# Performance work log

Hardware: AMD Instinct MI355X
Metric: run time of the kernel (lower is better)

## Reference

```python
import jax, jax.numpy as jnp
import numpy as np

EMBED_DIM = 1024
NUM_HEADS = 16
HEAD_DIM = EMBED_DIM // NUM_HEADS
KERNEL = 3
PAD = KERNEL // 2
B, L = 4, 1024


def conv1d(x, w, b):
    # x: [B, D, L], w: [D_out, D_in, K], b: [D_out]; 'same' padding like nn.Conv1d(padding=K//2)
    y = jax.lax.conv_general_dilated(
        x, w, window_strides=(1,), padding=[(PAD, PAD)],
        dimension_numbers=('NCH', 'OIH', 'NCH'))
    return y + b[None, :, None]


def setup_inputs() -> dict:
    key = jax.random.key(0)
    ks = jax.random.split(key, 12)
    fan = EMBED_DIM * KERNEL
    bound = 1.0 / np.sqrt(fan)
    def wconv(k):
        return jax.random.uniform(k, (EMBED_DIM, EMBED_DIM, KERNEL), jnp.float32, -bound, bound)
    def bconv(k):
        return jax.random.uniform(k, (EMBED_DIM,), jnp.float32, -bound, bound)
    return {
        'query': jax.random.normal(ks[0], (B, L, EMBED_DIM), jnp.float32),
        'key': jax.random.normal(ks[1], (B, L, EMBED_DIM), jnp.float32),
        'value': jax.random.normal(ks[2], (B, L, EMBED_DIM), jnp.float32),
        'key_padding_mask': jax.random.randint(ks[3], (B, L), 0, 2) > 0,
        'attn_mask': jnp.zeros((L, L), jnp.float32),
        'q_w': wconv(ks[4]), 'q_b': bconv(ks[5]),
        'k_w': wconv(ks[6]), 'k_b': bconv(ks[7]),
        'v_w': wconv(ks[8]), 'v_b': bconv(ks[9]),
        'o_w': wconv(ks[10]), 'o_b': bconv(ks[11]),
    }


def reference(query, key, value, key_padding_mask, attn_mask,
              q_w, q_b, k_w, k_b, v_w, v_b, o_w, o_b):
    scale = HEAD_DIM ** -0.5
    # projections: [B, D, L]
    q = conv1d(jnp.swapaxes(query, 1, 2), q_w, q_b)
    k = conv1d(jnp.swapaxes(key, 1, 2), k_w, k_b)
    v = conv1d(jnp.swapaxes(value, 1, 2), v_w, v_b)
    # [B, H, d, L]
    q = q.reshape(B, NUM_HEADS, HEAD_DIM, L)
    k = k.reshape(B, NUM_HEADS, HEAD_DIM, L)
    v = v.reshape(B, NUM_HEADS, HEAD_DIM, L)
    # scores: [B, H, L, L]
    scores = jnp.einsum('bhdi,bhdj->bhij', q, k) * scale
    scores = scores + attn_mask[None, None, :, :]
    scores = jnp.where(key_padding_mask[:, None, None, :], -jnp.inf, scores)
    attn = jax.nn.softmax(scores, axis=-1)  # dropout p=0 (eval) -> identity
    out = jnp.einsum('bhij,bhdj->bhdi', attn, v)  # [B, H, d, L]
    out = out.reshape(B, EMBED_DIM, L)
    out = conv1d(out, o_w, o_b)
    return jnp.swapaxes(out, 1, 2)  # [B, L, D]
```

## Files before the change

### kernel.cpp

```cpp
#include <hip/hip_runtime.h>
#include <math.h>

#define NB 4
#define NL 1024
#define ND 1024
#define NH 16
#define HD 64
#define PLN 4194304

typedef __attribute__((ext_vector_type(8))) short bf16x8;
typedef __attribute__((ext_vector_type(4))) float f32x4;

static __device__ __forceinline__ unsigned short f32_to_bf16(float f) {
  unsigned u = __float_as_uint(f);
  u += 0x7FFFu + ((u >> 16) & 1u);
  return (unsigned short)(u >> 16);
}
static __device__ __forceinline__ float bf16_to_f32(unsigned short s) {
  return __uint_as_float(((unsigned)s) << 16);
}
static __device__ __forceinline__ float exp2_f(float x) {
  float r;
  asm("v_exp_f32 %0, %1" : "=v"(r) : "v"(x));
  return r;
}

static __device__ __forceinline__ void split8(float4 a, float4 b, bf16x8* hi, bf16x8* lo) {
  unsigned u[8] = {__float_as_uint(a.x), __float_as_uint(a.y),
                   __float_as_uint(a.z), __float_as_uint(a.w),
                   __float_as_uint(b.x), __float_as_uint(b.y),
                   __float_as_uint(b.z), __float_as_uint(b.w)};
  union { unsigned p[4]; bf16x8 v; } H, L;
#pragma unroll
  for (int p = 0; p < 4; ++p) {
    unsigned u0 = u[2 * p], u1 = u[2 * p + 1];
    H.p[p] = __builtin_amdgcn_perm(u1, u0, 0x07060302u);
    unsigned l0 = __float_as_uint(__uint_as_float(u0) - __uint_as_float(u0 & 0xFFFF0000u));
    unsigned l1 = __float_as_uint(__uint_as_float(u1) - __uint_as_float(u1 & 0xFFFF0000u));
    L.p[p] = __builtin_amdgcn_perm(l1, l0, 0x07060302u);
  }
  *hi = H.v; *lo = L.v;
}

__global__ __launch_bounds__(256) void wcvt_kernel(
    const float* __restrict__ w0, const float* __restrict__ w1,
    const float* __restrict__ w2, const float* __restrict__ w3,
    unsigned short* __restrict__ wb, int* __restrict__ flag)
{
  if (blockIdx.x == 0 && blockIdx.y == 0 && threadIdx.x == 0) flag[0] = 0;
  const int t = blockIdx.y;
  const int o = blockIdx.x;
  const float* w = (t == 0) ? w0 : (t == 1) ? w1 : (t == 2) ? w2 : w3;
  unsigned short* hi = wb + (size_t)t * 6 * (1u << 20);
  unsigned short* lo = hi + 3 * (1u << 20);
  const int tid = threadIdx.x;
  float v[12];
  const float* src = w + (size_t)o * (ND * 3) + tid * 12;
#pragma unroll
  for (int j = 0; j < 3; ++j) {
    float4 f = *(const float4*)(src + j * 4);
    v[j * 4 + 0] = f.x; v[j * 4 + 1] = f.y; v[j * 4 + 2] = f.z; v[j * 4 + 3] = f.w;
  }
#pragma unroll
  for (int k = 0; k < 3; ++k) {
    unsigned short hh[4], ll[4];
#pragma unroll
    for (int ii = 0; ii < 4; ++ii) {
      float x = v[ii * 3 + k];
      unsigned short h = f32_to_bf16(x);
      float r = x - bf16_to_f32(h);
      hh[ii] = h; ll[ii] = f32_to_bf16(r);
    }
    size_t dst = (size_t)k * (ND * ND) + (size_t)o * ND + tid * 4;
    *(ushort4*)&hi[dst] = make_ushort4(hh[0], hh[1], hh[2], hh[3]);
    *(ushort4*)&lo[dst] = make_ushort4(ll[0], ll[1], ll[2], ll[3]);
  }
}

__global__ __launch_bounds__(256) void amask_scan(
    const float* __restrict__ a, int* __restrict__ flag)
{
  size_t i = ((size_t)blockIdx.x * 256 + threadIdx.x) * 4;
  float4 v = *(const float4*)&a[i];
  if (v.x != 0.f || v.y != 0.f || v.z != 0.f || v.w != 0.f) atomicOr(flag, 1);
}

__global__ __launch_bounds__(256) void xsplit_kernel(
    const float* __restrict__ x0, const float* __restrict__ x1,
    const float* __restrict__ x2, unsigned short* __restrict__ xs)
{
  const int z = blockIdx.y;
  const float* x = (z == 0) ? x0 : (z == 1) ? x1 : x2;
  const size_t i = ((size_t)blockIdx.x * 256 + threadIdx.x) * 8;
  float4 a = *(const float4*)&x[i];
  float4 b = *(const float4*)&x[i + 4];
  bf16x8 hi, lo;
  split8(a, b, &hi, &lo);
  unsigned short* ph = xs + (size_t)z * 2 * PLN;
  *(bf16x8*)&ph[i] = hi;
  *(bf16x8*)&ph[PLN + i] = lo;
}

template<int ASPLIT, int MODE>
__global__ __launch_bounds__(256, 3) void conv_mfma2(
    const void* X0v, const void* X1v, const void* X2v,
    const unsigned short* __restrict__ wb,
    const float* b0, const float* b1, const float* b2,
    float* Y0)
{
  __shared__ __align__(16) unsigned char Araw[16384];
  __shared__ unsigned short Bh[128 * 32];
  __shared__ unsigned short Bl[128 * 32];
  float* Af = (float*)Araw;
  unsigned short* Ah = (unsigned short*)Araw;
  unsigned short* Al = (unsigned short*)(Araw + 8192);

  const int tid = threadIdx.x, lane = tid & 63, wave = tid >> 6;
  const int lin = blockIdx.x + 8 * (blockIdx.y + 32 * blockIdx.z);
  const int g = lin & 7, t = lin >> 3;
  const int nb = (g & 3) * 2 + (t & 1);
  const int mb = (g >> 2) * 16 + ((t >> 1) & 15);
  const int z  = t >> 5;
  const int n0 = nb * 128, m0 = mb * 128;
  const int b = m0 >> 10, l0v = m0 & (NL - 1);

  const unsigned short* Wh = (MODE == 0) ? wb + (size_t)z * 6 * (1u << 20) : wb;
  const unsigned short* Wl = Wh + 3 * (1u << 20);

  const float* Xf = nullptr;
  const unsigned short* Xh_ = nullptr;
  const unsigned short* Xl_ = nullptr;
  if (ASPLIT) {
    const unsigned short* p = (const unsigned short*)((MODE == 0)
        ? (z == 0 ? X0v : (z == 1 ? X1v : X2v)) : X0v);
    Xh_ = p; Xl_ = p + PLN;
  } else {
    Xf = (const float*)((MODE == 0) ? (z == 0 ? X0v : (z == 1 ? X1v : X2v)) : X0v);
  }

  const int wm = (wave >> 1) * 64, wn = (wave & 1) * 64;
  const int mrow = lane & 15, quad = lane >> 4;
  const int r16 = lane >> 2, cs = lane & 3;
  const int src_chunk = (cs - (r16 >> 1)) & 3;
  const int bswz = ((quad + (mrow >> 1)) & 3) * 8;

  f32x4 acc[4][4] = {};

  const int kbeg = (MODE == 0) ? 0 : z;
  const int kend = (MODE == 0) ? 3 : z + 1;
  for (int koff = kbeg; koff < kend; ++koff) {
    const bool edge_lo = (l0v == 0 && koff == 0);
    const bool edge_hi = (l0v == NL - 128 && koff == 2);
    for (int i0 = 0; i0 < ND; i0 += 32) {
#pragma unroll
      for (int s = 0; s < 2; ++s) {
        const int seg = wave * 2 + s;
        const size_t goff = ((size_t)koff << 20) +
                            (size_t)(n0 + seg * 16 + r16) * ND + i0 + src_chunk * 8;
        __builtin_amdgcn_global_load_lds(
            (const __attribute__((address_space(1))) unsigned int*)(Wh + goff),
            (__attribute__((address_space(3))) unsigned int*)&Bh[seg * 512], 16, 0, 0);
        __builtin_amdgcn_global_load_lds(
            (const __attribute__((address_space(1))) unsigned int*)(Wl + goff),
            (__attribute__((address_space(3))) unsigned int*)&Bl[seg * 512], 16, 0, 0);
      }
      if (ASPLIT) {
#pragma unroll
        for (int j = 0; j < 4; ++j) {
          const int seg = wave * 2 + (j & 1);
          const int row = seg * 16 + (lane >> 2);
          const int slot = lane & 3;
          const int chunk = (slot - (row >> 1)) & 3;
          int l = l0v + row + koff - 1;
          l = (l < 0) ? 0 : (l > NL - 1 ? NL - 1 : l);
          const unsigned short* Xp = (j >> 1) ? Xl_ : Xh_;
          unsigned short* dst = ((j >> 1) ? Al : Ah) + seg * 512;
          const unsigned short* gp = Xp + ((size_t)(b << 10) + l) * ND + i0 + chunk * 8;
          __builtin_amdgcn_global_load_lds(
              (const __attribute__((address_space(1))) unsigned int*)gp,
              (__attribute__((address_space(3))) unsigned int*)dst, 16, 0, 0);
        }
      } else {
#pragma unroll
        for (int j = 0; j < 4; ++j) {
          const int s = (wave * 4 + j) * 64 + lane;
          const int row = s >> 3, sir = s & 7;
          const int chunk = (sir - (row & 7)) & 7;
          int l = l0v + row + koff - 1;
          l = (l < 0) ? 0 : (l > NL - 1 ? NL - 1 : l);
          const float* gp = Xf + ((size_t)(b << 10) + l) * ND + i0 + chunk * 4;
          __builtin_amdgcn_global_load_lds(
              (const __attribute__((address_space(1))) unsigned int*)gp,
              (__attribute__((address_space(3))) unsigned int*)&Af[(wave * 4 + j) * 256],
              16, 0, 0);
        }
      }
      __syncthreads();
      if (edge_lo || edge_hi) {
        const int er = edge_lo ? 0 : 127;
        if (ASPLIT) {
          if (tid < 16) {
            unsigned short* pl = (tid < 8) ? Ah : Al;
            *(ushort4*)&pl[er * 32 + (tid & 7) * 4] = make_ushort4(0, 0, 0, 0);
          }
        } else {
          if (tid < 8) *(float4*)&Af[er * 32 + tid * 4] = make_float4(0.f, 0.f, 0.f, 0.f);
        }
        __syncthreads();
      }
      bf16x8 ah[4], al[4];
      if (ASPLIT) {
#pragma unroll
        for (int mi = 0; mi < 4; ++mi) {
          const int row = wm + mi * 16 + mrow;
          const int cso = ((quad + (row >> 1)) & 3) * 8;
          ah[mi] = *(const bf16x8*)&Ah[row * 32 + cso];
          al[mi] = *(const bf16x8*)&Al[row * 32 + cso];
        }
      } else {
#pragma unroll
        for (int mi = 0; mi < 4; ++mi) {
          const int row = wm + mi * 16 + mrow, r7 = row & 7;
          float4 fa = *(const float4*)&Af[row * 32 + (((quad * 2) + r7) & 7) * 4];
          float4 fb = *(const float4*)&Af[row * 32 + (((quad * 2 + 1) + r7) & 7) * 4];
          split8(fa, fb, &ah[mi], &al[mi]);
        }
      }
#pragma unroll
      for (int ni = 0; ni < 4; ++ni) {
        const int brow = wn + ni * 16 + mrow;
        bf16x8 bh = *(const bf16x8*)&Bh[brow * 32 + bswz];
        bf16x8 bl = *(const bf16x8*)&Bl[brow * 32 + bswz];
#pragma unroll
        for (int mi = 0; mi < 4; ++mi) {
          acc[mi][ni] = __builtin_amdgcn_mfma_f32_16x16x32_bf16(ah[mi], bh, acc[mi][ni], 0, 0, 0);
          acc[mi][ni] = __builtin_amdgcn_mfma_f32_16x16x32_bf16(ah[mi], bl, acc[mi][ni], 0, 0, 0);
          acc[mi][ni] = __builtin_amdgcn_mfma_f32_16x16x32_bf16(al[mi], bh, acc[mi][ni], 0, 0, 0);
        }
      }
      __syncthreads();
    }
  }

  if (MODE == 0) {
    const float* bias = (z == 0) ? b0 : (z == 1) ? b1 : b2;
    unsigned short* U = (unsigned short*)Y0;
    if (z < 2) {
      unsigned short* Ph = U + (size_t)(2 * z) * PLN;
      unsigned short* Pl = Ph + PLN;
      const float sc = (z == 0) ? 0.18033688011112042f : 1.0f;
#pragma unroll
      for (int ni = 0; ni < 4; ++ni) {
        const int n = n0 + wn + ni * 16 + mrow;
        const float bv = bias[n];
        const int h = n >> 6, dd = n & 63;
        const int bh = b * NH + h;
#pragma unroll
        for (int mi = 0; mi < 4; ++mi) {
          const int mbase = m0 + wm + mi * 16 + quad * 4;
          f32x4 v = acc[mi][ni];
#pragma unroll
          for (int r = 0; r < 4; ++r) {
            const int l = (mbase + r) & (NL - 1);
            const float val = (v[r] + bv) * sc;
            const unsigned u = __float_as_uint(val);
            const unsigned short hh = (unsigned short)(u >> 16);
            const float res = val - __uint_as_float(u & 0xFFFF0000u);
            const unsigned short ll = (unsigned short)(__float_as_uint(res) >> 16);
            const size_t off = ((size_t)bh * NL + l) * HD + dd;
            Ph[off] = hh; Pl[off] = ll;
          }
        }
      }
    } else {
      unsigned short* Pv = U + (size_t)4 * PLN;
#pragma unroll
      for (int ni = 0; ni < 4; ++ni) {
        const int n = n0 + wn + ni * 16 + mrow;
        const float bv = bias[n];
        const int h = n >> 6, dd = n & 63;
        const int bh = b * NH + h;
#pragma unroll
        for (int mi = 0; mi < 4; ++mi) {
          const int mbase = m0 + wm + mi * 16 + quad * 4;
          const int lb = mbase & (NL - 1);
          f32x4 v = acc[mi][ni];
          ushort4 s4 = make_ushort4(f32_to_bf16(v[0] + bv), f32_to_bf16(v[1] + bv),
                                    f32_to_bf16(v[2] + bv), f32_to_bf16(v[3] + bv));
          *(ushort4*)&Pv[((size_t)bh * HD + dd) * NL + lb] = s4;
        }
      }
    }
  } else {
    float* P = Y0 + (size_t)z * ((size_t)NB * NL * ND);
#pragma unroll
    for (int ni = 0; ni < 4; ++ni) {
      const int n = n0 + wn + ni * 16 + mrow;
#pragma unroll
      for (int mi = 0; mi < 4; ++mi) {
        const int mbase = m0 + wm + mi * 16 + quad * 4;
        f32x4 v = acc[mi][ni];
#pragma unroll
        for (int r = 0; r < 4; ++r) {
          const int l = (mbase + r) & (NL - 1);
          P[((size_t)(b << 10) + l) * ND + n] = v[r];
        }
      }
    }
  }
}

__global__ __launch_bounds__(256) void reduce_kernel(
    const float* __restrict__ P, const float* __restrict__ bias, float* __restrict__ out)
{
  const size_t S = (size_t)NB * NL * ND;
  const size_t idx = ((size_t)blockIdx.x * 256 + threadIdx.x) * 4;
  const int n = (int)(idx & (ND - 1));
  float4 p0 = *(const float4*)&P[idx];
  float4 p1 = *(const float4*)&P[idx + S];
  float4 p2 = *(const float4*)&P[idx + 2 * S];
  float4 bv = *(const float4*)&bias[n];
  float4 r;
  r.x = p0.x + p1.x + p2.x + bv.x;
  r.y = p0.y + p1.y + p2.y + bv.y;
  r.z = p0.z + p1.z + p2.z + bv.z;
  r.w = p0.w + p1.w + p2.w + bv.w;
  *(float4*)&out[idx] = r;
}

__global__ __launch_bounds__(256, 3) void attn_mfma(
    const unsigned short* __restrict__ U, const int* __restrict__ kpm,
    const float* __restrict__ amask, const int* __restrict__ aflagp,
    unsigned short* __restrict__ AO)
{
  __shared__ __align__(16) unsigned short S[3 * 4096];
  __shared__ __align__(16) float Fm[NL];
  unsigned short* Kh = S;
  unsigned short* Kl = S + 4096;
  unsigned short* Vt = S + 8192;

  const int tid = threadIdx.x, lane = tid & 63, wave = tid >> 6;
  const int c = lane & 15, quad = lane >> 4;
  const int lin = blockIdx.x;
  const int bh = (lin & 7) + 8 * (lin >> 7);
  const int mt = (lin >> 3) & 15;
  const int b = bh >> 4;
  const int m0 = mt * 64;
  const int aflag = *aflagp;
  const int mrow = wave * 16 + c;
  const int gm = m0 + mrow;

  const size_t PLs = (size_t)PLN;
  const unsigned short* qTh = U;
  const unsigned short* qTl = U + PLs;
  const unsigned short* kTh = U + 2 * PLs;
  const unsigned short* kTl = U + 3 * PLs;
  const unsigned short* vTt = U + 4 * PLs;

  const int srow = lane >> 3;
  const int slot = lane & 7;
  const int chunk = (slot - srow) & 7;

#pragma unroll
  for (int q = 0; q < 4; ++q) {
    const int pl = q >> 1;
    const int i = wave * 2 + (q & 1);
    const int row = i * 8 + srow;
    const unsigned short* src = (pl ? qTl : qTh) +
        ((size_t)bh * NL + m0 + row) * HD + chunk * 8;
    unsigned short* dst = (pl ? Kl : Kh) + i * 512;
    __builtin_amdgcn_global_load_lds(
        (const __attribute__((address_space(1))) unsigned int*)src,
        (__attribute__((address_space(3))) unsigned int*)dst, 16, 0, 0);
  }
  {
    int4 kv = *(const int4*)&kpm[b * NL + tid * 4];
    float4 f;
    f.x = kv.x ? -INFINITY : 0.f;
    f.y = kv.y ? -INFINITY : 0.f;
    f.z = kv.z ? -INFINITY : 0.f;
    f.w = kv.w ? -INFINITY : 0.f;
    *(float4*)&Fm[tid * 4] = f;
  }
  __syncthreads();
  bf16x8 qbh[2], qbl[2];
#pragma unroll
  for (int kb = 0; kb < 2; ++kb) {
    const int cso = ((kb * 4 + quad + mrow) & 7) * 8;
    qbh[kb] = *(const bf16x8*)&Kh[mrow * 64 + cso];
    qbl[kb] = *(const bf16x8*)&Kl[mrow * 64 + cso];
  }

  f32x4 acc[4] = {};
  float m_r = -INFINITY, l_r = 0.0f;

  for (int n0t = 0; n0t < NL; n0t += 64) {
    __syncthreads();

#pragma unroll
    for (int q = 0; q < 6; ++q) {
      const int pl = q >> 1;
      const int i = wave * 2 + (q & 1);
      const int row = i * 8 + srow;
      const unsigned short* src;
      unsigned short* dst;
      if (pl == 0)      { src = kTh + ((size_t)bh * NL + n0t + row) * HD + chunk * 8; dst = Kh + i * 512; }
      else if (pl == 1) { src = kTl + ((size_t)bh * NL + n0t + row) * HD + chunk * 8; dst = Kl + i * 512; }
      else              { src = vTt + ((size_t)bh * HD + row) * NL + n0t + chunk * 8; dst = Vt + i * 512; }
      __builtin_amdgcn_global_load_lds(
          (const __attribute__((address_space(1))) unsigned int*)src,
          (__attribute__((address_space(3))) unsigned int*)dst, 16, 0, 0);
    }

    float mval[4][4];
#pragma unroll
    for (int nf = 0; nf < 4; ++nf) {
      float4 fm = *(const float4*)&Fm[n0t + nf * 16 + quad * 4];
      mval[nf][0] = fm.x; mval[nf][1] = fm.y; mval[nf][2] = fm.z; mval[nf][3] = fm.w;
    }
    if (aflag) {
#pragma unroll
      for (int nf = 0; nf < 4; ++nf)
#pragma unroll
        for (int r = 0; r < 4; ++r) {
          const int gn = n0t + nf * 16 + quad * 4 + r;
          mval[nf][r] += amask[(size_t)gm * NL + gn] * 1.4426950408889634f;
        }
    }
    __syncthreads();

    f32x4 sa[4] = {};
    __builtin_amdgcn_s_setprio(1);
#pragma unroll
    for (int kb = 0; kb < 2; ++kb)
#pragma unroll
      for (int nf = 0; nf < 4; ++nf) {
        const int row = nf * 16 + c;
        const int cso = ((kb * 4 + quad + row) & 7) * 8;
        bf16x8 kah = *(const bf16x8*)&Kh[row * 64 + cso];
        bf16x8 kal = *(const bf16x8*)&Kl[row * 64 + cso];
        sa[nf] = __builtin_amdgcn_mfma_f32_16x16x32_bf16(kah, qbh[kb], sa[nf], 0, 0, 0);
        sa[nf] = __builtin_amdgcn_mfma_f32_16x16x32_bf16(kah, qbl[kb], sa[nf], 0, 0, 0);
        sa[nf] = __builtin_amdgcn_mfma_f32_16x16x32_bf16(kal, qbh[kb], sa[nf], 0, 0, 0);
      }
    __builtin_amdgcn_s_setprio(0);

    float p[4][4];
    float tmax = -INFINITY;
#pragma unroll
    for (int nf = 0; nf < 4; ++nf)
#pragma unroll
      for (int r = 0; r < 4; ++r) {
        float s = sa[nf][r] + mval[nf][r];
        p[nf][r] = s;
        tmax = fmaxf(tmax, s);
      }
    tmax = fmaxf(tmax, __shfl_xor(tmax, 16));
    tmax = fmaxf(tmax, __shfl_xor(tmax, 32));
    float rs = 0.f;
    if (__all(tmax - m_r <= 8.0f)) {
      const float msafe = m_r;
#pragma unroll
      for (int nf = 0; nf < 4; ++nf)
#pragma unroll
        for (int r = 0; r < 4; ++r) {
          float e = exp2_f(p[nf][r] - msafe);
          p[nf][r] = e;
          rs += e;
        }
      rs += __shfl_xor(rs, 16);
      rs += __shfl_xor(rs, 32);
      l_r += rs;
    } else {
      const float newm = fmaxf(m_r, tmax);
      const float msafe = (newm == -INFINITY) ? 0.f : newm;
      const float alpha = exp2_f(m_r - msafe);
#pragma unroll
      for (int nf = 0; nf < 4; ++nf)
#pragma unroll
        for (int r = 0; r < 4; ++r) {
          float e = exp2_f(p[nf][r] - msafe);
          p[nf][r] = e;
          rs += e;
        }
      rs += __shfl_xor(rs, 16);
      rs += __shfl_xor(rs, 32);
      l_r = l_r * alpha + rs;
      m_r = newm;
#pragma unroll
      for (int df = 0; df < 4; ++df) {
        acc[df][0] *= alpha; acc[df][1] *= alpha;
        acc[df][2] *= alpha; acc[df][3] *= alpha;
      }
    }

    unsigned q16[4][2];
#pragma unroll
    for (int nf = 0; nf < 4; ++nf)
#pragma unroll
      for (int w = 0; w < 2; ++w)
        q16[nf][w] = (unsigned)f32_to_bf16(p[nf][2 * w]) |
                     ((unsigned)f32_to_bf16(p[nf][2 * w + 1]) << 16);

#pragma unroll
    for (int kb = 0; kb < 2; ++kb) {
      union { unsigned d[4]; bf16x8 v; } pb;
#pragma unroll
      for (int w = 0; w < 4; ++w) {
        const int addr = ((((quad & 1) * 2 + (w >> 1)) * 16 + c) << 2);
        unsigned v0 = __builtin_amdgcn_ds_bpermute(addr, (int)q16[2 * kb][w & 1]);
        unsigned v1 = __builtin_amdgcn_ds_bpermute(addr, (int)q16[2 * kb + 1][w & 1]);
        pb.d[w] = (quad >> 1) ? v1 : v0;
      }
      __builtin_amdgcn_s_setprio(1);
#pragma unroll
      for (int df = 0; df < 4; ++df) {
        const int row = df * 16 + c;
        const int cso = ((kb * 4 + quad + row) & 7) * 8;
        bf16x8 va = *(const bf16x8*)&Vt[row * 64 + cso];
        acc[df] = __builtin_amdgcn_mfma_f32_16x16x32_bf16(va, pb.v, acc[df], 0, 0, 0);
      }
      __builtin_amdgcn_s_setprio(0);
    }
  }

  __syncthreads();
  const float inv = 1.0f / l_r;
  float* Ob = (float*)S + wave * (16 * 68);
#pragma unroll
  for (int df = 0; df < 4; ++df)
#pragma unroll
    for (int r = 0; r < 4; ++r)
      Ob[c * 68 + df * 16 + quad * 4 + r] = acc[df][r] * inv;
  __syncthreads();
  const int mr2 = lane >> 2, cq2 = lane & 3;
  const int h = bh & 15;
  unsigned short* AOl_ = AO + PLN;
#pragma unroll
  for (int ii = 0; ii < 4; ++ii) {
    const int chunk2 = cq2 * 4 + ii;
    float4 v = *(const float4*)&Ob[mr2 * 68 + chunk2 * 4];
    const size_t off = ((size_t)(b << 10) + (m0 + wave * 16 + mr2)) * ND + h * HD + chunk2 * 4;
    float vv[4] = {v.x, v.y, v.z, v.w};
    ushort4 hh, ll;
    unsigned short* hp = (unsigned short*)&hh;
    unsigned short* lp = (unsigned short*)&ll;
#pragma unroll
    for (int e = 0; e < 4; ++e) {
      const unsigned u = __float_as_uint(vv[e]);
      hp[e] = (unsigned short)(u >> 16);
      const float res = vv[e] - __uint_as_float(u & 0xFFFF0000u);
      lp[e] = (unsigned short)(__float_as_uint(res) >> 16);
    }
    *(ushort4*)&AO[off] = hh;
    *(ushort4*)&AOl_[off] = ll;
  }
}

extern "C" void kernel_launch(void* const* d_in, const int* in_sizes, int n_in,
                              void* d_out, int out_size, void* d_ws, size_t ws_size,
                              hipStream_t stream) {
  (void)in_sizes; (void)n_in; (void)out_size;
  const float* query = (const float*)d_in[0];
  const float* key_  = (const float*)d_in[1];
  const float* value = (const float*)d_in[2];
  const int*   kpm   = (const int*)d_in[3];
  const float* amask = (const float*)d_in[4];
  const float* q_w = (const float*)d_in[5];
  const float* q_b = (const float*)d_in[6];
  const float* k_w = (const float*)d_in[7];
  const float* k_b = (const float*)d_in[8];
  const float* v_w = (const float*)d_in[9];
  const float* v_b = (const float*)d_in[10];
  const float* o_w = (const float*)d_in[11];
  const float* o_b = (const float*)d_in[12];
  float* out = (float*)d_out;

  unsigned short* Wb  = (unsigned short*)d_ws;
  unsigned short* U   = (unsigned short*)((char*)d_ws + (size_t)50331648);
  float*          P   = (float*)((char*)d_ws + (size_t)50331648);
  unsigned short* AOs = (unsigned short*)d_ws;
  unsigned short* Xs  = (unsigned short*)((char*)d_ws + (size_t)92274688);
  int* flag = (int*)d_out;
  const bool presplit = ws_size >= (size_t)142606336;

  wcvt_kernel<<<dim3(1024, 4), 256, 0, stream>>>(q_w, k_w, v_w, o_w, Wb, flag);
  amask_scan<<<1024, 256, 0, stream>>>(amask, flag);
  if (presplit) {
    xsplit_kernel<<<dim3(2048, 3), 256, 0, stream>>>(query, key_, value, Xs);
    conv_mfma2<1, 0><<<dim3(8, 32, 3), 256, 0, stream>>>(
        Xs, Xs + (size_t)2 * PLN, Xs + (size_t)4 * PLN, Wb, q_b, k_b, v_b, (float*)U);
  } else {
    conv_mfma2<0, 0><<<dim3(8, 32, 3), 256, 0, stream>>>(
        query, key_, value, Wb, q_b, k_b, v_b, (float*)U);
  }
  attn_mfma<<<1024, 256, 0, stream>>>(U, kpm, amask, flag, AOs);
  conv_mfma2<1, 1><<<dim3(8, 32, 3), 256, 0, stream>>>(
      AOs, AOs, AOs, Wb + (size_t)3 * 6 * (1u << 20), o_b, o_b, o_b, P);
  reduce_kernel<<<4096, 256, 0, stream>>>(P, o_b, out);
}
```

Measured before the change: 518.5 us.

## Double-buffer LDS tiles in conv and attention kernels to overlap loads

Both the conv GEMM kernel and the attention kernel now use two LDS buffers, so the global-to-LDS copy for the next tile is issued before computing on the current one. Each iteration needs one barrier instead of two. In the conv kernel the boundary-row zeroing moves from an LDS store plus extra barrier to register masking of the A fragments. The conv kernel's LDS doubles to 64KB and its launch bound drops from 3 to 2 blocks per CU, which lowers occupancy in exchange for the overlap.

```diff
diff --git a/kernel.cpp b/kernel.cpp
--- a/kernel.cpp
+++ b/kernel.cpp
@@ -102,18 +102,13 @@
 }
 
 template<int ASPLIT, int MODE>
-__global__ __launch_bounds__(256, 3) void conv_mfma2(
+__global__ __launch_bounds__(256, 2) void conv_mfma3(
     const void* X0v, const void* X1v, const void* X2v,
     const unsigned short* __restrict__ wb,
     const float* b0, const float* b1, const float* b2,
     float* Y0)
 {
-  __shared__ __align__(16) unsigned char Araw[16384];
-  __shared__ unsigned short Bh[128 * 32];
-  __shared__ unsigned short Bl[128 * 32];
-  float* Af = (float*)Araw;
-  unsigned short* Ah = (unsigned short*)Araw;
-  unsigned short* Al = (unsigned short*)(Araw + 8192);
+  __shared__ __align__(16) unsigned char LDSb[2][32768];
 
   const int tid = threadIdx.x, lane = tid & 63, wave = tid >> 6;
   const int lin = blockIdx.x + 8 * (blockIdx.y + 32 * blockIdx.z);
@@ -130,7 +125,7 @@
   const float* Xf = nullptr;
   const unsigned short* Xh_ = nullptr;
   const unsigned short* Xl_ = nullptr;
-  if (ASPLIT) {
+  if constexpr (ASPLIT) {
     const unsigned short* p = (const unsigned short*)((MODE == 0)
         ? (z == 0 ? X0v : (z == 1 ? X1v : X2v)) : X0v);
     Xh_ = p; Xl_ = p + PLN;
@@ -144,102 +139,115 @@
   const int src_chunk = (cs - (r16 >> 1)) & 3;
   const int bswz = ((quad + (mrow >> 1)) & 3) * 8;
 
+  const int NSTEP = (MODE == 0) ? 96 : 32;
+
+  auto stage = [&](int s, int buf) {
+    const int koff = (MODE == 0) ? (s >> 5) : z;
+    const int i0 = ((MODE == 0) ? (s & 31) : s) << 5;
+    unsigned short* BhD = (unsigned short*)(LDSb[buf] + 16384);
+    unsigned short* BlD = (unsigned short*)(LDSb[buf] + 24576);
+#pragma unroll
+    for (int s2 = 0; s2 < 2; ++s2) {
+      const int seg = wave * 2 + s2;
+      const size_t goff = ((size_t)koff << 20) +
+                          (size_t)(n0 + seg * 16 + r16) * ND + i0 + src_chunk * 8;
+      __builtin_amdgcn_global_load_lds(
+          (const __attribute__((address_space(1))) unsigned int*)(Wh + goff),
+          (__attribute__((address_space(3))) unsigned int*)&BhD[seg * 512], 16, 0, 0);
+      __builtin_amdgcn_global_load_lds(
+          (const __attribute__((address_space(1))) unsigned int*)(Wl + goff),
+          (__attribute__((address_space(3))) unsigned int*)&BlD[seg * 512], 16, 0, 0);
+    }
+    if constexpr (ASPLIT) {
+      unsigned short* AhD = (unsigned short*)(LDSb[buf]);
+      unsigned short* AlD = (unsigned short*)(LDSb[buf] + 8192);
+#pragma unroll
+      for (int j = 0; j < 4; ++j) {
+        const int seg = wave * 2 + (j & 1);
+        const int row = seg * 16 + (lane >> 2);
+        const int slot = lane & 3;
+        const int chunk = (slot - (row >> 1)) & 3;
+        int l = l0v + row + koff - 1;
+        l = (l < 0) ? 0 : (l > NL - 1 ? NL - 1 : l);
+        const unsigned short* Xp = (j >> 1) ? Xl_ : Xh_;
+        unsigned short* dst = ((j >> 1) ? AlD : AhD) + seg * 512;
+        const unsigned short* gp = Xp + ((size_t)(b << 10) + l) * ND + i0 + chunk * 8;
+        __builtin_amdgcn_global_load_lds(
+            (const __attribute__((address_space(1))) unsigned int*)gp,
+            (__attribute__((address_space(3))) unsigned int*)dst, 16, 0, 0);
+      }
+    } else {
+      float* AfD = (float*)(LDSb[buf]);
+#pragma unroll
+      for (int j = 0; j < 4; ++j) {
+        const int s2 = (wave * 4 + j) * 64 + lane;
+        const int row = s2 >> 3, sir = s2 & 7;
+        const int chunk = (sir - (row & 7)) & 7;
+        int l = l0v + row + koff - 1;
+        l = (l < 0) ? 0 : (l > NL - 1 ? NL - 1 : l);
+        const float* gp = Xf + ((size_t)(b << 10) + l) * ND + i0 + chunk * 4;
+        __builtin_amdgcn_global_load_lds(
+            (const __attribute__((address_space(1))) unsigned int*)gp,
+            (__attribute__((address_space(3))) unsigned int*)&AfD[(wave * 4 + j) * 256],
+            16, 0, 0);
+      }
+    }
+  };
+
   f32x4 acc[4][4] = {};
-
-  const int kbeg = (MODE == 0) ? 0 : z;
-  const int kend = (MODE == 0) ? 3 : z + 1;
-  for (int koff = kbeg; koff < kend; ++koff) {
-    const bool edge_lo = (l0v == 0 && koff == 0);
-    const bool edge_hi = (l0v == NL - 128 && koff == 2);
-    for (int i0 = 0; i0 < ND; i0 += 32) {
-#pragma unroll
-      for (int s = 0; s < 2; ++s) {
-        const int seg = wave * 2 + s;
-        const size_t goff = ((size_t)koff << 20) +
-                            (size_t)(n0 + seg * 16 + r16) * ND + i0 + src_chunk * 8;
-        __builtin_amdgcn_global_load_lds(
-            (const __attribute__((address_space(1))) unsigned int*)(Wh + goff),
-            (__attribute__((address_space(3))) unsigned int*)&Bh[seg * 512], 16, 0, 0);
-        __builtin_amdgcn_global_load_lds(
-            (const __attribute__((address_space(1))) unsigned int*)(Wl + goff),
-            (__attribute__((address_space(3))) unsigned int*)&Bl[seg * 512], 16, 0, 0);
-      }
-      if (ASPLIT) {
-#pragma unroll
-        for (int j = 0; j < 4; ++j) {
-          const int seg = wave * 2 + (j & 1);
-          const int row = seg * 16 + (lane >> 2);
-          const int slot = lane & 3;
-          const int chunk = (slot - (row >> 1)) & 3;
-          int l = l0v + row + koff - 1;
-          l = (l < 0) ? 0 : (l > NL - 1 ? NL - 1 : l);
-          const unsigned short* Xp = (j >> 1) ? Xl_ : Xh_;
-          unsigned short* dst = ((j >> 1) ? Al : Ah) + seg * 512;
-          const unsigned short* gp = Xp + ((size_t)(b << 10) + l) * ND + i0 + chunk * 8;
-          __builtin_amdgcn_global_load_lds(
-              (const __attribute__((address_space(1))) unsigned int*)gp,
-              (__attribute__((address_space(3))) unsigned int*)dst, 16, 0, 0);
-        }
-      } else {
-#pragma unroll
-        for (int j = 0; j < 4; ++j) {
-          const int s = (wave * 4 + j) * 64 + lane;
-          const int row = s >> 3, sir = s & 7;
-          const int chunk = (sir - (row & 7)) & 7;
-          int l = l0v + row + koff - 1;
-          l = (l < 0) ? 0 : (l > NL - 1 ? NL - 1 : l);
-          const float* gp = Xf + ((size_t)(b << 10) + l) * ND + i0 + chunk * 4;
-          __builtin_amdgcn_global_load_lds(
-              (const __attribute__((address_space(1))) unsigned int*)gp,
-              (__attribute__((address_space(3))) unsigned int*)&Af[(wave * 4 + j) * 256],
-              16, 0, 0);
-        }
-      }
-      __syncthreads();
-      if (edge_lo || edge_hi) {
-        const int er = edge_lo ? 0 : 127;
-        if (ASPLIT) {
-          if (tid < 16) {
-            unsigned short* pl = (tid < 8) ? Ah : Al;
-            *(ushort4*)&pl[er * 32 + (tid & 7) * 4] = make_ushort4(0, 0, 0, 0);
-          }
-        } else {
-          if (tid < 8) *(float4*)&Af[er * 32 + tid * 4] = make_float4(0.f, 0.f, 0.f, 0.f);
-        }
-        __syncthreads();
-      }
-      bf16x8 ah[4], al[4];
-      if (ASPLIT) {
-#pragma unroll
-        for (int mi = 0; mi < 4; ++mi) {
-          const int row = wm + mi * 16 + mrow;
-          const int cso = ((quad + (row >> 1)) & 3) * 8;
-          ah[mi] = *(const bf16x8*)&Ah[row * 32 + cso];
-          al[mi] = *(const bf16x8*)&Al[row * 32 + cso];
-        }
-      } else {
-#pragma unroll
-        for (int mi = 0; mi < 4; ++mi) {
-          const int row = wm + mi * 16 + mrow, r7 = row & 7;
-          float4 fa = *(const float4*)&Af[row * 32 + (((quad * 2) + r7) & 7) * 4];
-          float4 fb = *(const float4*)&Af[row * 32 + (((quad * 2 + 1) + r7) & 7) * 4];
-          split8(fa, fb, &ah[mi], &al[mi]);
-        }
-      }
-#pragma unroll
-      for (int ni = 0; ni < 4; ++ni) {
-        const int brow = wn + ni * 16 + mrow;
-        bf16x8 bh = *(const bf16x8*)&Bh[brow * 32 + bswz];
-        bf16x8 bl = *(const bf16x8*)&Bl[brow * 32 + bswz];
-#pragma unroll
-        for (int mi = 0; mi < 4; ++mi) {
-          acc[mi][ni] = __builtin_amdgcn_mfma_f32_16x16x32_bf16(ah[mi], bh, acc[mi][ni], 0, 0, 0);
-          acc[mi][ni] = __builtin_amdgcn_mfma_f32_16x16x32_bf16(ah[mi], bl, acc[mi][ni], 0, 0, 0);
-          acc[mi][ni] = __builtin_amdgcn_mfma_f32_16x16x32_bf16(al[mi], bh, acc[mi][ni], 0, 0, 0);
-        }
-      }
-      __syncthreads();
-    }
+  const bf16x8 zz = {};
+
+  stage(0, 0);
+  __syncthreads();
+  int cur = 0;
+  for (int s = 0; s < NSTEP; ++s) {
+    if (s + 1 < NSTEP) stage(s + 1, cur ^ 1);
+
+    const int koff = (MODE == 0) ? (s >> 5) : z;
+    const bool e_lo = (l0v == 0 && koff == 0);
+    const bool e_hi = (l0v == NL - 128 && koff == 2);
+
+    bf16x8 ah[4], al[4];
+    if constexpr (ASPLIT) {
+      const unsigned short* Ah = (const unsigned short*)(LDSb[cur]);
+      const unsigned short* Al = (const unsigned short*)(LDSb[cur] + 8192);
+#pragma unroll
+      for (int mi = 0; mi < 4; ++mi) {
+        const int row = wm + mi * 16 + mrow;
+        const int cso = ((quad + (row >> 1)) & 3) * 8;
+        ah[mi] = *(const bf16x8*)&Ah[row * 32 + cso];
+        al[mi] = *(const bf16x8*)&Al[row * 32 + cso];
+        const bool kill = (e_lo && row == 0) || (e_hi && row == 127);
+        if (kill) { ah[mi] = zz; al[mi] = zz; }
+      }
+    } else {
+      const float* Af = (const float*)(LDSb[cur]);
+#pragma unroll
+      for (int mi = 0; mi < 4; ++mi) {
+        const int row = wm + mi * 16 + mrow, r7 = row & 7;
+        float4 fa = *(const float4*)&Af[row * 32 + (((quad * 2) + r7) & 7) * 4];
+        float4 fb = *(const float4*)&Af[row * 32 + (((quad * 2 + 1) + r7) & 7) * 4];
+        split8(fa, fb, &ah[mi], &al[mi]);
+        const bool kill = (e_lo && row == 0) || (e_hi && row == 127);
+        if (kill) { ah[mi] = zz; al[mi] = zz; }
+      }
+    }
+    const unsigned short* BhC = (const unsigned short*)(LDSb[cur] + 16384);
+    const unsigned short* BlC = (const unsigned short*)(LDSb[cur] + 24576);
+#pragma unroll
+    for (int ni = 0; ni < 4; ++ni) {
+      const int brow = wn + ni * 16 + mrow;
+      bf16x8 bh = *(const bf16x8*)&BhC[brow * 32 + bswz];
+      bf16x8 bl = *(const bf16x8*)&BlC[brow * 32 + bswz];
+#pragma unroll
+      for (int mi = 0; mi < 4; ++mi) {
+        acc[mi][ni] = __builtin_amdgcn_mfma_f32_16x16x32_bf16(ah[mi], bh, acc[mi][ni], 0, 0, 0);
+        acc[mi][ni] = __builtin_amdgcn_mfma_f32_16x16x32_bf16(ah[mi], bl, acc[mi][ni], 0, 0, 0);
+        acc[mi][ni] = __builtin_amdgcn_mfma_f32_16x16x32_bf16(al[mi], bh, acc[mi][ni], 0, 0, 0);
+      }
+    }
+    __syncthreads();
+    cur ^= 1;
   }
 
   if (MODE == 0) {
@@ -333,11 +341,8 @@
     const float* __restrict__ amask, const int* __restrict__ aflagp,
     unsigned short* __restrict__ AO)
 {
-  __shared__ __align__(16) unsigned short S[3 * 4096];
+  __shared__ __align__(16) unsigned short S[2][3 * 4096];
   __shared__ __align__(16) float Fm[NL];
-  unsigned short* Kh = S;
-  unsigned short* Kl = S + 4096;
-  unsigned short* Vt = S + 8192;
 
   const int tid = threadIdx.x, lane = tid & 63, wave = tid >> 6;
   const int c = lane & 15, quad = lane >> 4;
@@ -361,6 +366,26 @@
   const int slot = lane & 7;
   const int chunk = (slot - srow) & 7;
 
+  auto stage_tile = [&](int n0t, unsigned short* B) {
+    unsigned short* KhD = B;
+    unsigned short* KlD = B + 4096;
+    unsigned short* VtD = B + 8192;
+#pragma unroll
+    for (int q = 0; q < 6; ++q) {
+      const int pl = q >> 1;
+      const int i = wave * 2 + (q & 1);
+      const int row = i * 8 + srow;
+      const unsigned short* src;
+      unsigned short* dst;
+      if (pl == 0)      { src = kTh + ((size_t)bh * NL + n0t + row) * HD + chunk * 8; dst = KhD + i * 512; }
+      else if (pl == 1) { src = kTl + ((size_t)bh * NL + n0t + row) * HD + chunk * 8; dst = KlD + i * 512; }
+      else              { src = vTt + ((size_t)bh * HD + row) * NL + n0t + chunk * 8; dst = VtD + i * 512; }
+      __builtin_amdgcn_global_load_lds(
+          (const __attribute__((address_space(1))) unsigned int*)src,
+          (__attribute__((address_space(3))) unsigned int*)dst, 16, 0, 0);
+    }
+  };
+
 #pragma unroll
   for (int q = 0; q < 4; ++q) {
     const int pl = q >> 1;
@@ -368,7 +393,7 @@
     const int row = i * 8 + srow;
     const unsigned short* src = (pl ? qTl : qTh) +
         ((size_t)bh * NL + m0 + row) * HD + chunk * 8;
-    unsigned short* dst = (pl ? Kl : Kh) + i * 512;
+    unsigned short* dst = (pl ? (S[0] + 4096) : S[0]) + i * 512;
     __builtin_amdgcn_global_load_lds(
         (const __attribute__((address_space(1))) unsigned int*)src,
         (__attribute__((address_space(3))) unsigned int*)dst, 16, 0, 0);
@@ -387,30 +412,23 @@
 #pragma unroll
   for (int kb = 0; kb < 2; ++kb) {
     const int cso = ((kb * 4 + quad + mrow) & 7) * 8;
-    qbh[kb] = *(const bf16x8*)&Kh[mrow * 64 + cso];
-    qbl[kb] = *(const bf16x8*)&Kl[mrow * 64 + cso];
-  }
+    qbh[kb] = *(const bf16x8*)&S[0][mrow * 64 + cso];
+    qbl[kb] = *(const bf16x8*)&S[0][4096 + mrow * 64 + cso];
+  }
+  stage_tile(0, S[1]);
+  __syncthreads();
 
   f32x4 acc[4] = {};
   float m_r = -INFINITY, l_r = 0.0f;
-
-  for (int n0t = 0; n0t < NL; n0t += 64) {
-    __syncthreads();
-
-#pragma unroll
-    for (int q = 0; q < 6; ++q) {
-      const int pl = q >> 1;
-      const int i = wave * 2 + (q & 1);
-      const int row = i * 8 + srow;
-      const unsigned short* src;
-      unsigned short* dst;
-      if (pl == 0)      { src = kTh + ((size_t)bh * NL + n0t + row) * HD + chunk * 8; dst = Kh + i * 512; }
-      else if (pl == 1) { src = kTl + ((size_t)bh * NL + n0t + row) * HD + chunk * 8; dst = Kl + i * 512; }
-      else              { src = vTt + ((size_t)bh * HD + row) * NL + n0t + chunk * 8; dst = Vt + i * 512; }
-      __builtin_amdgcn_global_load_lds(
-          (const __attribute__((address_space(1))) unsigned int*)src,
-          (__attribute__((address_space(3))) unsigned int*)dst, 16, 0, 0);
-    }
+  int cur = 1;
+
+  for (int tt = 0; tt < 16; ++tt) {
+    const int n0t = tt * 64;
+    if (tt < 15) stage_tile(n0t + 64, S[cur ^ 1]);
+
+    const unsigned short* Kh = S[cur];
+    const unsigned short* Kl = S[cur] + 4096;
+    const unsigned short* Vt = S[cur] + 8192;
 
     float mval[4][4];
 #pragma unroll
@@ -427,7 +445,6 @@
           mval[nf][r] += amask[(size_t)gm * NL + gn] * 1.4426950408889634f;
         }
     }
-    __syncthreads();
 
     f32x4 sa[4] = {};
     __builtin_amdgcn_s_setprio(1);
@@ -522,11 +539,12 @@
       }
       __builtin_amdgcn_s_setprio(0);
     }
-  }
-
-  __syncthreads();
+    __syncthreads();
+    cur ^= 1;
+  }
+
   const float inv = 1.0f / l_r;
-  float* Ob = (float*)S + wave * (16 * 68);
+  float* Ob = (float*)S[0] + wave * (16 * 68);
 #pragma unroll
   for (int df = 0; df < 4; ++df)
 #pragma unroll
@@ -588,14 +606,14 @@
   amask_scan<<<1024, 256, 0, stream>>>(amask, flag);
   if (presplit) {
     xsplit_kernel<<<dim3(2048, 3), 256, 0, stream>>>(query, key_, value, Xs);
-    conv_mfma2<1, 0><<<dim3(8, 32, 3), 256, 0, stream>>>(
+    conv_mfma3<1, 0><<<dim3(8, 32, 3), 256, 0, stream>>>(
         Xs, Xs + (size_t)2 * PLN, Xs + (size_t)4 * PLN, Wb, q_b, k_b, v_b, (float*)U);
   } else {
-    conv_mfma2<0, 0><<<dim3(8, 32, 3), 256, 0, stream>>>(
+    conv_mfma3<0, 0><<<dim3(8, 32, 3), 256, 0, stream>>>(
         query, key_, value, Wb, q_b, k_b, v_b, (float*)U);
   }
   attn_mfma<<<1024, 256, 0, stream>>>(U, kpm, amask, flag, AOs);
-  conv_mfma2<1, 1><<<dim3(8, 32, 3), 256, 0, stream>>>(
+  conv_mfma3<1, 1><<<dim3(8, 32, 3), 256, 0, stream>>>(
       AOs, AOs, AOs, Wb + (size_t)3 * 6 * (1u << 20), o_b, o_b, o_b, P);
   reduce_kernel<<<4096, 256, 0, stream>>>(P, o_b, out);
 }
```

New measurement: 548.8 us. +5.8%, slower.
